# Optimization experiments

Hardware: AMD Instinct MI355X
Metric: run time of the kernel (lower is better)

Reference implementation:

```python
import jax, jax.numpy as jnp
import numpy as np

IMG = 128          # image_size
TEX = 4            # texture_size (hard-coded in module)
WIDTH = float(np.tan(np.radians(30.0)))  # nr default viewing_angle=30
NEAR = 0.1
# images dict: values are [distance, azimuth, elevation]; eye = get_points_from_angles(dist, elev, azim)
VIEWS = [(2.83, 45.0, 0.0), (2.0, 0.0, 90.0), (3.46, 45.0, 45.0), (3.0, 0.0, 0.0)]  # (dist, elev, azim)


def _eye_from_angles(dist, elev_deg, azim_deg):
    e, a = np.radians(elev_deg), np.radians(azim_deg)
    return jnp.asarray([dist * np.cos(e) * np.sin(a), dist * np.sin(e), -dist * np.cos(e) * np.cos(a)], jnp.float32)


def _normalize(v):
    return v / jnp.linalg.norm(v)


def _trilinear(tex, c):
    # tex: [P, T, T, T, 3], c: [P, 3] continuous coords in [0, T-1]
    i0 = jnp.clip(jnp.floor(c).astype(jnp.int32), 0, TEX - 2)
    f = c - i0.astype(c.dtype)
    pi = jnp.arange(tex.shape[0])
    out = jnp.zeros((tex.shape[0], 3), tex.dtype)
    for dx in (0, 1):
        for dy in (0, 1):
            for dz in (0, 1):
                wgt = ((f[:, 0] if dx else 1.0 - f[:, 0])
                       * (f[:, 1] if dy else 1.0 - f[:, 1])
                       * (f[:, 2] if dz else 1.0 - f[:, 2]))
                out = out + wgt[:, None] * tex[pi, i0[:, 0] + dx, i0[:, 1] + dy, i0[:, 2] + dz]
    return out


def _render(verts, faces, tex, eye):
    # verts [V,3], faces [F,3] int, tex [F,T,T,T,3] -> image [1,3,IMG,IMG]
    # look_at transform (at=origin, up=+y)
    z_ax = _normalize(-eye)
    x_ax = _normalize(jnp.cross(jnp.asarray([0.0, 1.0, 0.0], jnp.float32), z_ax))
    y_ax = _normalize(jnp.cross(z_ax, x_ax))
    R = jnp.stack([x_ax, y_ax, z_ax])                       # [3,3]
    v = (verts - eye) @ R.T                                 # [V,3]
    # perspective projection
    z = v[:, 2]
    v = jnp.stack([v[:, 0] / (z * WIDTH), v[:, 1] / (z * WIDTH), z], -1)
    fv = v[faces]                                           # [F,3,3]

    # pixel grid in NDC [-1,1], row 0 = top
    s = (jnp.arange(IMG, dtype=jnp.float32) + 0.5) / IMG * 2.0 - 1.0
    px = jnp.broadcast_to(s[None, :], (IMG, IMG)).ravel()
    py = jnp.broadcast_to(-s[:, None], (IMG, IMG)).ravel()
    p = jnp.stack([px, py], -1)                             # [P,2]

    v0 = fv[:, 0, :2]
    e1 = fv[:, 1, :2] - v0
    e2 = fv[:, 2, :2] - v0
    det = e1[:, 0] * e2[:, 1] - e1[:, 1] * e2[:, 0]         # [F]
    ok = jnp.abs(det) > 1e-8
    inv_det = jnp.where(ok, 1.0 / jnp.where(ok, det, 1.0), 0.0)
    d = p[None, :, :] - v0[:, None, :]                      # [F,P,2]
    w1 = (e2[:, None, 1] * d[..., 0] - e2[:, None, 0] * d[..., 1]) * inv_det[:, None]
    w2 = (-e1[:, None, 1] * d[..., 0] + e1[:, None, 0] * d[..., 1]) * inv_det[:, None]
    w0 = 1.0 - w1 - w2
    fz = fv[:, :, 2]                                        # [F,3]
    depth = w0 * fz[:, 0:1] + w1 * fz[:, 1:2] + w2 * fz[:, 2:3]  # [F,P]
    visible = (w0 >= 0) & (w1 >= 0) & (w2 >= 0) & ok[:, None] & (depth > NEAR)
    depth_m = jnp.where(visible, depth, jnp.inf)
    fidx = jnp.argmin(depth_m, axis=0)                      # [P]
    P = fidx.shape[0]
    pi = jnp.arange(P)
    hit = jnp.isfinite(depth_m[fidx, pi])
    wsel = jnp.stack([w0[fidx, pi], w1[fidx, pi], w2[fidx, pi]], -1)  # [P,3]
    coords = jnp.clip(wsel, 0.0, 1.0) * (TEX - 1)
    color = _trilinear(tex[fidx], coords) * hit[:, None].astype(tex.dtype)  # [P,3]
    return color.reshape(IMG, IMG, 3).transpose(2, 0, 1)[None]  # [1,3,IMG,IMG]


def setup_inputs() -> dict:
    key = jax.random.key(0)
    k1, k2, k3, k4 = jax.random.split(key, 4)
    V, F = 1024, 1024
    vertices = jax.random.normal(k1, (1, V, 3), jnp.float32) * 0.5
    faces = jax.random.randint(k2, (1, F, 3), 0, V, jnp.int32)
    textures = jax.random.normal(k3, (1, F, TEX, TEX, TEX, 3), jnp.float32)
    image_refs = jax.random.uniform(k4, (4, 1, IMG, IMG), jnp.float32)
    return {"vertices": vertices, "faces": faces, "textures": textures, "image_refs": image_refs}


def reference(vertices, faces, textures, image_refs):
    tex = jnp.tanh(textures)[0]   # [F,T,T,T,3]
    verts = vertices[0]
    fcs = faces[0]
    loss = jnp.float32(0.0)
    for c, (dist, elev, azim) in enumerate(VIEWS):
        image = _render(verts, fcs, tex, _eye_from_angles(dist, elev, azim))  # [1,3,H,W]
        ref = image_refs[c][:, None]                                          # [1,1,H,W]
        loss = loss + jnp.sum((image - ref) ** 2)
    return loss
```

## Files before the change

### kernel.cpp

```cpp
#include <hip/hip_runtime.h>
#include <math.h>

#define IMG 128
#define NPIX (IMG * IMG)
#define NF 1024
#define NCHUNK 8
#define CHF 128
#define NEAR_Z 0.1f
#define DY 0.015625f

struct AllViews { float m[4][12]; };

__device__ __forceinline__ float fast_tanh(float x)
{
    float xc = fminf(fmaxf(x, -10.0f), 10.0f);
    float e = __expf(2.0f * xc);
    return __fdividef(e - 1.0f, e + 1.0f);
}

__global__ void precompute(const float* __restrict__ verts,
                           const int* __restrict__ faces,
                           float4* __restrict__ fd,
                           unsigned int* __restrict__ counter,
                           AllViews vc, float W)
{
    int t = blockIdx.x * blockDim.x + threadIdx.x;
    if (t == 0) *counter = 0;
    if (t >= 4 * NF) return;
    int view = t >> 10, f = t & (NF - 1);
    const float* M = vc.m[view];

    float proj[3][3];
#pragma unroll
    for (int k = 0; k < 3; ++k) {
        int vi = faces[f * 3 + k];
        float px = verts[vi * 3 + 0] - M[9];
        float py = verts[vi * 3 + 1] - M[10];
        float pz = verts[vi * 3 + 2] - M[11];
        float x = M[0] * px + M[1] * py + M[2] * pz;
        float y = M[3] * px + M[4] * py + M[5] * pz;
        float z = M[6] * px + M[7] * py + M[8] * pz;
        proj[k][0] = x / (z * W);
        proj[k][1] = y / (z * W);
        proj[k][2] = z;
    }
    float v0x = proj[0][0], v0y = proj[0][1];
    float e1x = proj[1][0] - v0x, e1y = proj[1][1] - v0y;
    float e2x = proj[2][0] - v0x, e2y = proj[2][1] - v0y;
    float det = e1x * e2y - e1y * e2x;
    bool ok = fabsf(det) > 1e-8f;
    float inv = ok ? 1.0f / det : 0.0f;
    float a1x = e2y * inv, a1y = -e2x * inv;
    float b1 = -(a1x * v0x + a1y * v0y);
    float a2x = -e1y * inv, a2y = e1x * inv;
    float b2 = -(a2x * v0x + a2y * v0y);
    float z0 = ok ? proj[0][2] : 0.0f;
    float g1 = proj[1][2] - proj[0][2];
    float g2 = proj[2][2] - proj[0][2];
    float ymin = INFINITY, ymax = -INFINITY;
    if (ok) {
        ymin = fminf(fminf(proj[0][1], proj[1][1]), proj[2][1]);
        ymax = fmaxf(fmaxf(proj[0][1], proj[1][1]), proj[2][1]);
    }
    float4* o = fd + (size_t)t * 3;
    o[0] = make_float4(a1x, a1y, b1, a2x);
    o[1] = make_float4(a2y, b2, z0, g1);
    o[2] = make_float4(g2, ymin, ymax, 0.0f);
}

__global__ __launch_bounds__(256) void raster(
    const float4* __restrict__ fd,
    unsigned long long* __restrict__ keys)
{
    __shared__ float4 lds4[CHF * 3];
    __shared__ unsigned long long MASK[4][2];

    int bid = blockIdx.x;
    int view  = bid >> 7;
    int b     = bid & 127;
    int chunk = b & (NCHUNK - 1);
    int strip = b >> 3;
    int tid  = threadIdx.x;
    int wave = tid >> 6, lane = tid & 63;

    const float4* src = fd + (size_t)(view * NF + chunk * CHF) * 3;
    for (int i = tid; i < CHF * 3; i += 256) lds4[i] = src[i];
    __syncthreads();

    if (wave < 2) {
        float4 bb = lds4[(wave * 64 + lane) * 3 + 2];
#pragma unroll
        for (int rp = 0; rp < 4; ++rp) {
            int r0 = strip * 8 + 2 * rp;
            float syhi = 1.0f - (r0 + 0.5f) * DY;
            float sylo = syhi - DY;
            unsigned long long m = __ballot((bb.y <= syhi) && (bb.z >= sylo));
            if (lane == 0) MASK[rp][wave] = m;
        }
    }
    __syncthreads();

    int r0 = strip * 8 + 2 * wave;
    float sy0 = 1.0f - (r0 + 0.5f) * DY;
    float sx0 = (lane + 0.5f) * DY - 1.0f;

    float bst[4] = {INFINITY, INFINITY, INFINITY, INFINITY};
    int   bfi[4] = {0, 0, 0, 0};
    const float* ldsf = (const float*)lds4;

#pragma unroll
    for (int half = 0; half < 2; ++half) {
        unsigned long long m = MASK[wave][half];
        int fbase = half * 64;
        while (m) {
            int f = fbase + (int)__builtin_ctzll(m);
            m &= m - 1;
            float4 q0 = lds4[f * 3 + 0];
            float4 q1 = lds4[f * 3 + 1];
            float g2  = ldsf[f * 12 + 8];
            float w1_00 = fmaf(q0.x, sx0, fmaf(q0.y, sy0, q0.z));
            float w2_00 = fmaf(q0.w, sx0, fmaf(q1.x, sy0, q1.y));
            float w1_01 = w1_00 + q0.x;
            float w2_01 = w2_00 + q0.w;
            float w1_10 = fmaf(q0.y, -DY, w1_00);
            float w2_10 = fmaf(q1.x, -DY, w2_00);
            float w1_11 = w1_10 + q0.x;
            float w2_11 = w2_10 + q0.w;
            float w1q[4] = {w1_00, w1_01, w1_10, w1_11};
            float w2q[4] = {w2_00, w2_01, w2_10, w2_11};
#pragma unroll
            for (int q = 0; q < 4; ++q) {
                float w1 = w1q[q], w2 = w2q[q];
                float dep = fmaf(w2, g2, fmaf(w1, q1.w, q1.z));
                bool vis = (fminf(w1, w2) >= 0.0f) && (w1 + w2 <= 1.0f) &&
                           (dep > NEAR_Z);
                bool take = vis && (dep < bst[q]);
                bst[q] = take ? dep : bst[q];
                bfi[q] = take ? f : bfi[q];
            }
        }
    }

    size_t base = ((size_t)(view * NCHUNK + chunk) << 14);
    int p00 = r0 * IMG + lane;
    int fo = chunk * CHF;
#pragma unroll
    for (int q = 0; q < 4; ++q) {
        unsigned long long key =
            ((unsigned long long)__float_as_uint(bst[q]) << 32) |
            (unsigned int)(fo + bfi[q]);
        keys[base + p00 + (q & 1) * 64 + (q >> 1) * IMG] = key;
    }
}

__global__ __launch_bounds__(256) void shade_loss(
    const float4* __restrict__ fd,
    const unsigned long long* __restrict__ keys,
    const float* __restrict__ tex,
    const float* __restrict__ refs,
    float* __restrict__ partial, unsigned int* __restrict__ counter,
    float* __restrict__ out)
{
    __shared__ float wsum[4];
    __shared__ bool last;
    int tid = threadIdx.x;
    int t = blockIdx.x * 256 + tid;
    int view = t >> 14, p = t & (NPIX - 1);
    int row = p >> 7, col = p & 127;
    float sx = (col + 0.5f) * DY - 1.0f;
    float sy = 1.0f - (row + 0.5f) * DY;

    const unsigned long long* kb = keys + ((size_t)(view * NCHUNK) << 14) + p;
    unsigned long long key = ~0ULL;
#pragma unroll
    for (int c = 0; c < NCHUNK; ++c) {
        unsigned long long k = kb[(size_t)c << 14];
        key = (k < key) ? k : key;
    }

    bool hit = (unsigned int)(key >> 32) < 0x7f800000u;
    float ref = refs[t];
    float lossv;
    if (hit) {
        int f = (int)(key & 0xffffffffu);
        const float4* Q = fd + (size_t)(view * NF + f) * 3;
        float4 q0 = Q[0];
        float4 q1 = Q[1];
        float w1 = fmaf(q0.x, sx, fmaf(q0.y, sy, q0.z));
        float w2 = fmaf(q0.w, sx, fmaf(q1.x, sy, q1.y));
        float w0 = 1.0f - w1 - w2;
        float cx = fminf(fmaxf(w0, 0.0f), 1.0f) * 3.0f;
        float cy = fminf(fmaxf(w1, 0.0f), 1.0f) * 3.0f;
        float cz = fminf(fmaxf(w2, 0.0f), 1.0f) * 3.0f;
        int ix = min(max((int)floorf(cx), 0), 2);
        int iy = min(max((int)floorf(cy), 0), 2);
        int iz = min(max((int)floorf(cz), 0), 2);
        float fx = cx - (float)ix, fy = cy - (float)iy, fz = cz - (float)iz;

        const float* T = tex + (size_t)f * 192;
        float c0 = 0.0f, c1 = 0.0f, c2 = 0.0f;
#pragma unroll
        for (int dxi = 0; dxi < 2; ++dxi)
#pragma unroll
            for (int dyi = 0; dyi < 2; ++dyi)
#pragma unroll
                for (int dzi = 0; dzi < 2; ++dzi) {
                    float w = (dxi ? fx : 1.0f - fx) *
                              (dyi ? fy : 1.0f - fy) *
                              (dzi ? fz : 1.0f - fz);
                    int base = (((ix + dxi) * 4 + (iy + dyi)) * 4 + (iz + dzi)) * 3;
                    c0 += w * fast_tanh(T[base + 0]);
                    c1 += w * fast_tanh(T[base + 1]);
                    c2 += w * fast_tanh(T[base + 2]);
                }
        float d0 = c0 - ref, d1 = c1 - ref, d2 = c2 - ref;
        lossv = d0 * d0 + d1 * d1 + d2 * d2;
    } else {
        lossv = 3.0f * ref * ref;
    }

    for (int off = 32; off; off >>= 1) lossv += __shfl_down(lossv, off);
    if ((tid & 63) == 0) wsum[tid >> 6] = lossv;
    __syncthreads();
    if (tid == 0) {
        partial[blockIdx.x] = wsum[0] + wsum[1] + wsum[2] + wsum[3];
        __threadfence();
        unsigned int old = atomicAdd(counter, 1);
        last = (old == (unsigned int)(gridDim.x - 1));
    }
    __syncthreads();
    if (last) {
        __threadfence();
        float v = partial[tid];
        for (int off = 32; off; off >>= 1) v += __shfl_down(v, off);
        if ((tid & 63) == 0) wsum[tid >> 6] = v;
        __syncthreads();
        if (tid == 0) out[0] = wsum[0] + wsum[1] + wsum[2] + wsum[3];
    }
}

static void make_view(double dist, double elev, double azim, float* M)
{
    double e = elev * M_PI / 180.0, a = azim * M_PI / 180.0;
    float ex = (float)(dist * cos(e) * sin(a));
    float ey = (float)(dist * sin(e));
    float ez = (float)(-dist * cos(e) * cos(a));
    float zx = -ex, zy = -ey, zz = -ez;
    float n = sqrtf(zx * zx + zy * zy + zz * zz);
    zx /= n; zy /= n; zz /= n;
    float xx = zz, xy = 0.0f, xz = -zx;
    n = sqrtf(xx * xx + xy * xy + xz * xz);
    xx /= n; xy /= n; xz /= n;
    float yx = zy * xz - zz * xy;
    float yy = zz * xx - zx * xz;
    float yz = zx * xy - zy * xx;
    n = sqrtf(yx * yx + yy * yy + yz * yz);
    yx /= n; yy /= n; yz /= n;
    M[0] = xx; M[1] = xy; M[2] = xz;
    M[3] = yx; M[4] = yy; M[5] = yz;
    M[6] = zx; M[7] = zy; M[8] = zz;
    M[9] = ex; M[10] = ey; M[11] = ez;
}

extern "C" void kernel_launch(void* const* d_in, const int* in_sizes, int n_in,
                              void* d_out, int out_size, void* d_ws, size_t ws_size,
                              hipStream_t stream)
{
    const float* verts = (const float*)d_in[0];
    const int*   faces = (const int*)d_in[1];
    const float* tex   = (const float*)d_in[2];
    const float* refs  = (const float*)d_in[3];
    float* out = (float*)d_out;

    char* ws = (char*)d_ws;
    float4* fd = (float4*)ws;
    ws += (size_t)4 * NF * 3 * sizeof(float4);
    unsigned long long* keys = (unsigned long long*)ws;
    ws += (size_t)4 * NCHUNK * NPIX * sizeof(unsigned long long);
    float* partial = (float*)ws;
    ws += 256 * sizeof(float);
    unsigned int* counter = (unsigned int*)ws;

    AllViews vc;
    const double V[4][3] = {{2.83, 45.0, 0.0}, {2.0, 0.0, 90.0},
                            {3.46, 45.0, 45.0}, {3.0, 0.0, 0.0}};
    for (int i = 0; i < 4; ++i) make_view(V[i][0], V[i][1], V[i][2], vc.m[i]);
    float W = (float)tan(M_PI / 6.0);

    precompute<<<16, 256, 0, stream>>>(verts, faces, fd, counter, vc, W);
    raster<<<512, 256, 0, stream>>>(fd, keys);
    shade_loss<<<256, 256, 0, stream>>>(fd, keys, tex, refs,
                                        partial, counter, out);
}
```

Before: 48.77 us.

## Rasterize 16x16 tiles with 2D bbox culling and compacted face lists

After: 44.47 us. -8.8%, faster.

```diff
diff --git a/kernel.cpp b/kernel.cpp
--- a/kernel.cpp
+++ b/kernel.cpp
@@ -1,11 +1,12 @@
 #include <hip/hip_runtime.h>
+#include <hip/hip_fp16.h>
 #include <math.h>
 
 #define IMG 128
 #define NPIX (IMG * IMG)
 #define NF 1024
-#define NCHUNK 8
-#define CHF 128
+#define NCHUNK 4
+#define CHF 256
 #define NEAR_Z 0.1f
 #define DY 0.015625f
 
@@ -57,29 +58,39 @@
     float z0 = ok ? proj[0][2] : 0.0f;
     float g1 = proj[1][2] - proj[0][2];
     float g2 = proj[2][2] - proj[0][2];
-    float ymin = INFINITY, ymax = -INFINITY;
+    float ddx = ok ? (g1 * a1x + g2 * a2x) : 0.0f;
+    float ddy = ok ? (g1 * a1y + g2 * a2y) : 0.0f;
+    float dc  = ok ? (z0 + g1 * b1 + g2 * b2) : 0.0f;
+
+    float xmin = INFINITY, xmax = -INFINITY, ymin = INFINITY, ymax = -INFINITY;
     if (ok) {
+        xmin = fminf(fminf(proj[0][0], proj[1][0]), proj[2][0]);
+        xmax = fmaxf(fmaxf(proj[0][0], proj[1][0]), proj[2][0]);
         ymin = fminf(fminf(proj[0][1], proj[1][1]), proj[2][1]);
         ymax = fmaxf(fmaxf(proj[0][1], proj[1][1]), proj[2][1]);
     }
+    __half2 hx = __halves2half2(__float2half_rd(xmin), __float2half_ru(xmax));
+    __half2 hy = __halves2half2(__float2half_rd(ymin), __float2half_ru(ymax));
+
     float4* o = fd + (size_t)t * 3;
-    o[0] = make_float4(a1x, a1y, b1, a2x);
-    o[1] = make_float4(a2y, b2, z0, g1);
-    o[2] = make_float4(g2, ymin, ymax, 0.0f);
-}
-
-__global__ __launch_bounds__(256) void raster(
+    o[0] = make_float4(a1x, a1y, b1, ddx);
+    o[1] = make_float4(a2x, a2y, b2, ddy);
+    o[2] = make_float4(dc, __uint_as_float(*(unsigned int*)&hx),
+                           __uint_as_float(*(unsigned int*)&hy), 0.0f);
+}
+
+__global__ __launch_bounds__(256, 4) void raster(
     const float4* __restrict__ fd,
     unsigned long long* __restrict__ keys)
 {
     __shared__ float4 lds4[CHF * 3];
-    __shared__ unsigned long long MASK[4][2];
+    __shared__ unsigned short list[4][CHF];
 
     int bid = blockIdx.x;
-    int view  = bid >> 7;
-    int b     = bid & 127;
+    int view  = bid >> 8;
+    int b     = bid & 255;
     int chunk = b & (NCHUNK - 1);
-    int strip = b >> 3;
+    int tile  = b >> 2;
     int tid  = threadIdx.x;
     int wave = tid >> 6, lane = tid & 63;
 
@@ -87,70 +98,59 @@
     for (int i = tid; i < CHF * 3; i += 256) lds4[i] = src[i];
     __syncthreads();
 
-    if (wave < 2) {
-        float4 bb = lds4[(wave * 64 + lane) * 3 + 2];
-#pragma unroll
-        for (int rp = 0; rp < 4; ++rp) {
-            int r0 = strip * 8 + 2 * rp;
-            float syhi = 1.0f - (r0 + 0.5f) * DY;
-            float sylo = syhi - DY;
-            unsigned long long m = __ballot((bb.y <= syhi) && (bb.z >= sylo));
-            if (lane == 0) MASK[rp][wave] = m;
-        }
-    }
-    __syncthreads();
-
-    int r0 = strip * 8 + 2 * wave;
-    float sy0 = 1.0f - (r0 + 0.5f) * DY;
-    float sx0 = (lane + 0.5f) * DY - 1.0f;
-
-    float bst[4] = {INFINITY, INFINITY, INFINITY, INFINITY};
-    int   bfi[4] = {0, 0, 0, 0};
+    int tr = (tile >> 3) * 16 + (wave >> 1) * 8;
+    int tc = (tile & 7) * 16 + (wave & 1) * 8;
+    int r  = tr + (lane >> 3);
+    int c  = tc + (lane & 7);
+    float sx = (c + 0.5f) * DY - 1.0f;
+    float sy = 1.0f - (r + 0.5f) * DY;
+    float cx0 = (tc + 0.5f) * DY - 1.0f;
+    float cx1 = (tc + 7.5f) * DY - 1.0f;
+    float syHi = 1.0f - (tr + 0.5f) * DY;
+    float syLo = 1.0f - (tr + 7.5f) * DY;
+
+    int cnt = 0;
+#pragma unroll
+    for (int word = 0; word < 4; ++word) {
+        int fi = word * 64 + lane;
+        float4 q2 = lds4[fi * 3 + 2];
+        unsigned int bxu = __float_as_uint(q2.y);
+        unsigned int byu = __float_as_uint(q2.z);
+        __half2 hx = *(__half2*)&bxu;
+        __half2 hy = *(__half2*)&byu;
+        float xmin = __low2float(hx),  xmax = __high2float(hx);
+        float ymin = __low2float(hy),  ymax = __high2float(hy);
+        bool inter = (xmin <= cx1) && (xmax >= cx0) &&
+                     (ymin <= syHi) && (ymax >= syLo);
+        unsigned long long m = __ballot(inter);
+        int prefix = __popcll(m & ((1ull << lane) - 1ull));
+        if (inter) list[wave][cnt + prefix] = (unsigned short)fi;
+        cnt += (int)__popcll(m);
+    }
+
+    float best = INFINITY;
+    int bf = 0;
     const float* ldsf = (const float*)lds4;
-
-#pragma unroll
-    for (int half = 0; half < 2; ++half) {
-        unsigned long long m = MASK[wave][half];
-        int fbase = half * 64;
-        while (m) {
-            int f = fbase + (int)__builtin_ctzll(m);
-            m &= m - 1;
-            float4 q0 = lds4[f * 3 + 0];
-            float4 q1 = lds4[f * 3 + 1];
-            float g2  = ldsf[f * 12 + 8];
-            float w1_00 = fmaf(q0.x, sx0, fmaf(q0.y, sy0, q0.z));
-            float w2_00 = fmaf(q0.w, sx0, fmaf(q1.x, sy0, q1.y));
-            float w1_01 = w1_00 + q0.x;
-            float w2_01 = w2_00 + q0.w;
-            float w1_10 = fmaf(q0.y, -DY, w1_00);
-            float w2_10 = fmaf(q1.x, -DY, w2_00);
-            float w1_11 = w1_10 + q0.x;
-            float w2_11 = w2_10 + q0.w;
-            float w1q[4] = {w1_00, w1_01, w1_10, w1_11};
-            float w2q[4] = {w2_00, w2_01, w2_10, w2_11};
-#pragma unroll
-            for (int q = 0; q < 4; ++q) {
-                float w1 = w1q[q], w2 = w2q[q];
-                float dep = fmaf(w2, g2, fmaf(w1, q1.w, q1.z));
-                bool vis = (fminf(w1, w2) >= 0.0f) && (w1 + w2 <= 1.0f) &&
-                           (dep > NEAR_Z);
-                bool take = vis && (dep < bst[q]);
-                bst[q] = take ? dep : bst[q];
-                bfi[q] = take ? f : bfi[q];
-            }
-        }
-    }
-
-    size_t base = ((size_t)(view * NCHUNK + chunk) << 14);
-    int p00 = r0 * IMG + lane;
-    int fo = chunk * CHF;
-#pragma unroll
-    for (int q = 0; q < 4; ++q) {
-        unsigned long long key =
-            ((unsigned long long)__float_as_uint(bst[q]) << 32) |
-            (unsigned int)(fo + bfi[q]);
-        keys[base + p00 + (q & 1) * 64 + (q >> 1) * IMG] = key;
-    }
+#pragma unroll 2
+    for (int i = 0; i < cnt; ++i) {
+        int f = list[wave][i];
+        float4 q0 = lds4[f * 3 + 0];
+        float4 q1 = lds4[f * 3 + 1];
+        float dc  = ldsf[f * 12 + 8];
+        float w1  = fmaf(q0.x, sx, fmaf(q0.y, sy, q0.z));
+        float w2  = fmaf(q1.x, sx, fmaf(q1.y, sy, q1.z));
+        float dep = fmaf(q0.w, sx, fmaf(q1.w, sy, dc));
+        bool vis  = (fminf(w1, w2) >= 0.0f) && (w1 + w2 <= 1.0f) &&
+                    (dep > NEAR_Z);
+        bool take = vis && (dep < best);
+        best = take ? dep : best;
+        bf   = take ? f : bf;
+    }
+
+    unsigned long long key =
+        ((unsigned long long)__float_as_uint(best) << 32) |
+        (unsigned int)(chunk * CHF + bf);
+    keys[((size_t)(view * NCHUNK + chunk) << 14) + r * IMG + c] = key;
 }
 
 __global__ __launch_bounds__(256) void shade_loss(
@@ -187,7 +187,7 @@
         float4 q0 = Q[0];
         float4 q1 = Q[1];
         float w1 = fmaf(q0.x, sx, fmaf(q0.y, sy, q0.z));
-        float w2 = fmaf(q0.w, sx, fmaf(q1.x, sy, q1.y));
+        float w2 = fmaf(q1.x, sx, fmaf(q1.y, sy, q1.z));
         float w0 = 1.0f - w1 - w2;
         float cx = fminf(fmaxf(w0, 0.0f), 1.0f) * 3.0f;
         float cy = fminf(fmaxf(w1, 0.0f), 1.0f) * 3.0f;
@@ -288,7 +288,7 @@
     float W = (float)tan(M_PI / 6.0);
 
     precompute<<<16, 256, 0, stream>>>(verts, faces, fd, counter, vc, W);
-    raster<<<512, 256, 0, stream>>>(fd, keys);
+    raster<<<1024, 256, 0, stream>>>(fd, keys);
     shade_loss<<<256, 256, 0, stream>>>(fd, keys, tex, refs,
                                         partial, counter, out);
 }
```
